# Optimization experiments

Hardware: AMD Instinct MI355X
Metric: run time of the kernel (lower is better)

## Reference

```python
import jax, jax.numpy as jnp
import numpy as np

EPS = 1e-5

@jax.custom_vjp
def sign_ste(x):
    # BinActivation / weight binarization: sign(x) in {-1,+1}
    return jnp.where(x >= 0, 1.0, -1.0).astype(x.dtype)

def _sign_fwd(x):
    return sign_ste(x), x

def _sign_bwd(x, g):
    # straight-through estimator with hardtanh clipping: pass grad where |x| <= 1
    return (g * (jnp.abs(x) <= 1.0).astype(g.dtype),)

sign_ste.defvjp(_sign_fwd, _sign_bwd)

def setup_inputs() -> dict:
    key = jax.random.key(0)
    k1, k2 = jax.random.split(key)
    x = jax.random.normal(k1, (32, 256, 56, 56), dtype=jnp.float32)
    W = jax.random.normal(k2, (256, 256, 3, 3), dtype=jnp.float32) * 0.1
    gamma = jnp.ones((256,), dtype=jnp.float32)
    beta = jnp.zeros((256,), dtype=jnp.float32)
    return {"x": x, "W": W, "gamma": gamma, "beta": beta}

def reference(x, W, gamma, beta):
    # binarize activation and weights to {-1,+1}
    xb = sign_ste(x)
    wb = sign_ste(W)
    # conv: NCHW x OIHW -> NCHW, stride 1, padding 1, dilation 1, no bias
    y = jax.lax.conv_general_dilated(
        xb, wb,
        window_strides=(1, 1),
        padding=[(1, 1), (1, 1)],
        rhs_dilation=(1, 1),
        dimension_numbers=("NCHW", "OIHW", "NCHW"),
    )
    # BatchNorm2d in training mode: batch statistics over (N,H,W), affine
    mean = jnp.mean(y, axis=(0, 2, 3), keepdims=True)          # [1,C,1,1]
    var = jnp.mean((y - mean) ** 2, axis=(0, 2, 3), keepdims=True)
    y = (y - mean) * jax.lax.rsqrt(var + EPS)
    y = y * gamma[None, :, None, None] + beta[None, :, None, None]
    # Hardtanh(-1, 1)
    return jnp.clip(y, -1.0, 1.0)
```

## Files before the change

### kernel.cpp

```cpp
#include <hip/hip_runtime.h>
#include <stdint.h>
#include <math.h>

#define N_IMG 32
#define C_IN  256
#define HW    56
#define P_PIX (HW*HW)
#define OC    256
#define WPC   8
#define NPIX  (N_IMG*P_PIX)
#define NTOT  ((double)N_IMG*(double)P_PIX)

__global__ __launch_bounds__(256) void pack_x_kernel(const float* __restrict__ x,
                                                     uint32_t* __restrict__ px,
                                                     uint32_t* __restrict__ zero_row) {
    if (blockIdx.x == 392) {
        if (threadIdx.x < 224) ((uint2*)zero_row)[threadIdx.x] = make_uint2(0u, 0u);
        return;
    }
    int lane = threadIdx.x & 63;
    int wh   = threadIdx.x >> 6;
    int pq   = blockIdx.x * 64 + lane;
    int n    = pq / 784;
    int q    = pq - n * 784;
    const float* xp = x + ((size_t)(n * C_IN + wh * 64)) * P_PIX + q * 4;
    uint32_t b0[4] = {0, 0, 0, 0};
    uint32_t b1[4] = {0, 0, 0, 0};
#pragma unroll 8
    for (int i = 0; i < 32; ++i) {
        float4 v = *(const float4*)(xp + (size_t)i * P_PIX);
        uint32_t bit = 1u << i;
        b0[0] |= (v.x >= 0.0f) ? bit : 0u;
        b0[1] |= (v.y >= 0.0f) ? bit : 0u;
        b0[2] |= (v.z >= 0.0f) ? bit : 0u;
        b0[3] |= (v.w >= 0.0f) ? bit : 0u;
    }
#pragma unroll 8
    for (int i = 0; i < 32; ++i) {
        float4 v = *(const float4*)(xp + (size_t)(i + 32) * P_PIX);
        uint32_t bit = 1u << i;
        b1[0] |= (v.x >= 0.0f) ? bit : 0u;
        b1[1] |= (v.y >= 0.0f) ? bit : 0u;
        b1[2] |= (v.z >= 0.0f) ? bit : 0u;
        b1[3] |= (v.w >= 0.0f) ? bit : 0u;
    }
    uint32_t* dst = px + ((size_t)(n * P_PIX + q * 4)) * WPC + wh * 2;
    *(uint2*)(dst + 0)  = make_uint2(b0[0], b1[0]);
    *(uint2*)(dst + 8)  = make_uint2(b0[1], b1[1]);
    *(uint2*)(dst + 16) = make_uint2(b0[2], b1[2]);
    *(uint2*)(dst + 24) = make_uint2(b0[3], b1[3]);
}

__global__ void pack_w_kernel(const float* __restrict__ Wt,
                              uint32_t* __restrict__ wp,
                              int* __restrict__ corr,
                              long long* __restrict__ sums,
                              long long* __restrict__ sumsq) {
    __shared__ int lpop[72];
    __shared__ int ltap[9];
    int o = blockIdx.x;
    int t = threadIdx.x;
    if (t == 0) { sums[o] = 0; sumsq[o] = 0; }
    if (t < 72) {
        int tap = t >> 3;
        int word = t & 7;
        const float* wpr = Wt + ((size_t)(o * C_IN + word * 32)) * 9 + tap;
        uint32_t bits = 0;
#pragma unroll
        for (int k = 0; k < 32; ++k) {
            float v = wpr[(size_t)k * 9];
            bits |= (v >= 0.0f) ? (1u << k) : 0u;
        }
        wp[o * 72 + t] = bits;
        lpop[t] = __popc(bits);
    }
    __syncthreads();
    if (t < 9) {
        int s = 0;
#pragma unroll
        for (int w = 0; w < 8; ++w) s += lpop[t * 8 + w];
        ltap[t] = s;
    }
    __syncthreads();
    if (t < 9) {
        int vc = t / 3, hc = t % 3;
        int c = 0;
        for (int dy = -1; dy <= 1; ++dy)
            for (int dx = -1; dx <= 1; ++dx) {
                bool inv = (dy == -1 && vc == 1) || (dy == 1 && vc == 2) ||
                           (dx == -1 && hc == 1) || (dx == 1 && hc == 2);
                if (inv) {
                    int tap = (dy + 1) * 3 + (dx + 1);
                    c += 256 - 2 * ltap[tap];
                }
            }
        corr[o * 9 + t] = c;
    }
}

#define LOADCOL(S, c) do {                                                    \
    int _c = (c);                                                             \
    const uint32_t* _p0 = ((unsigned)_c < 56u) ? (r0 + _c * 8) : zero_row;    \
    const uint32_t* _p1 = ((unsigned)_c < 56u) ? (r1 + _c * 8) : zero_row;    \
    const uint32_t* _p2 = ((unsigned)_c < 56u) ? (r2 + _c * 8) : zero_row;    \
    x0##S##a = *(const uint4*)_p0; x0##S##b = *(const uint4*)(_p0 + 4);       \
    x1##S##a = *(const uint4*)_p1; x1##S##b = *(const uint4*)(_p1 + 4);       \
    x2##S##a = *(const uint4*)_p2; x2##S##b = *(const uint4*)(_p2 + 4);       \
} while (0)

#define TAP(va, vb, t)                                                        \
    a0 += __popc((va).x ^ wreg[(t)*8+0]); a1 += __popc((va).y ^ wreg[(t)*8+1]); \
    a2 += __popc((va).z ^ wreg[(t)*8+2]); a3 += __popc((va).w ^ wreg[(t)*8+3]); \
    a0 += __popc((vb).x ^ wreg[(t)*8+4]); a1 += __popc((vb).y ^ wreg[(t)*8+5]); \
    a2 += __popc((vb).z ^ wreg[(t)*8+6]); a3 += __popc((vb).w ^ wreg[(t)*8+7]);

#define STEP(M, Cc, P, w, yptr) do {                                          \
    int a0 = 0, a1 = 0, a2 = 0, a3 = 0;                                       \
    TAP(x0##M##a,  x0##M##b,  0) TAP(x0##Cc##a, x0##Cc##b, 1) TAP(x0##P##a, x0##P##b, 2) \
    TAP(x1##M##a,  x1##M##b,  3) TAP(x1##Cc##a, x1##Cc##b, 4) TAP(x1##P##a, x1##P##b, 5) \
    TAP(x2##M##a,  x2##M##b,  6) TAP(x2##Cc##a, x2##Cc##b, 7) TAP(x2##P##a, x2##P##b, 8) \
    int acc = (a0 + a1) + (a2 + a3);                                          \
    int cr  = ((w) == 0) ? crL : (((w) == HW - 1) ? crR : crM);               \
    int v   = 2304 - 2 * acc - cr;                                            \
    *(yptr) = (short)v;                                                       \
    s += v; q += __mul24(v, v);                                               \
    LOADCOL(M, (w) + 3);                                                      \
} while (0)

__global__ __launch_bounds__(256, 2) void bconv_kernel(const uint32_t* __restrict__ px,
                                                       const uint32_t* __restrict__ wp,
                                                       const int* __restrict__ corr,
                                                       const uint32_t* __restrict__ zero_row,
                                                       short* __restrict__ y16t,
                                                       long long* __restrict__ sums,
                                                       long long* __restrict__ sumsq) {
    int o   = threadIdx.x;
    int blk = blockIdx.x;
    int n = blk / HW, h = blk - n * HW;

    uint32_t wreg[72];
    {
        const uint4* wq = (const uint4*)(wp + o * 72);
#pragma unroll
        for (int j = 0; j < 18; ++j) {
            uint4 t4 = wq[j];
            wreg[4*j+0] = t4.x; wreg[4*j+1] = t4.y;
            wreg[4*j+2] = t4.z; wreg[4*j+3] = t4.w;
        }
    }
    int vc  = (h == 0) ? 1 : ((h == HW - 1) ? 2 : 0);
    int crM = corr[o * 9 + vc * 3 + 0];
    int crL = corr[o * 9 + vc * 3 + 1];
    int crR = corr[o * 9 + vc * 3 + 2];

    const uint32_t* rowb = px + (size_t)(n * P_PIX) * WPC;
    const uint32_t* r0 = (h > 0)      ? rowb + (h - 1) * HW * WPC : zero_row;
    const uint32_t* r1 = rowb + h * HW * WPC;
    const uint32_t* r2 = (h < HW - 1) ? rowb + (h + 1) * HW * WPC : zero_row;

    uint4 x0Aa, x0Ab, x1Aa, x1Ab, x2Aa, x2Ab;
    uint4 x0Ba, x0Bb, x1Ba, x1Bb, x2Ba, x2Bb;
    uint4 x0Ca, x0Cb, x1Ca, x1Cb, x2Ca, x2Cb;
    uint4 x0Da, x0Db, x1Da, x1Db, x2Da, x2Db;

    LOADCOL(A, -1);
    LOADCOL(B, 0);
    LOADCOL(C, 1);
    LOADCOL(D, 2);

    short* yw = y16t + ((size_t)(n * P_PIX + h * HW)) * OC + o;
    int s = 0, q = 0;

    for (int wb = 0; wb < HW; wb += 4) {
        STEP(A, B, C, wb + 0, yw);
        STEP(B, C, D, wb + 1, yw + OC);
        STEP(C, D, A, wb + 2, yw + 2 * OC);
        STEP(D, A, B, wb + 3, yw + 3 * OC);
        yw += 4 * OC;
    }

    atomicAdd((unsigned long long*)&sums[o],  (unsigned long long)(long long)s);
    atomicAdd((unsigned long long*)&sumsq[o], (unsigned long long)(long long)q);
}

__global__ __launch_bounds__(256) void apply_kernel(const short* __restrict__ y16t,
                                                    float* __restrict__ out,
                                                    const long long* __restrict__ sums,
                                                    const long long* __restrict__ sumsq,
                                                    const float* __restrict__ gamma,
                                                    const float* __restrict__ beta) {
    __shared__ float sbf[512];
    __shared__ uint32_t tile[64 * 129];
    int t = threadIdx.x;
    {
        int o = t;
        double invN = 1.0 / NTOT;
        double mean = (double)sums[o] * invN;
        double var  = (double)sumsq[o] * invN - mean * mean;
        double sc   = (double)gamma[o] / sqrt(var + 1e-5);
        sbf[o]       = (float)sc;
        sbf[256 + o] = (float)((double)beta[o] - mean * sc);
    }
    int blk = blockIdx.x;
    int n   = blk / 49;
    int pl0 = (blk - n * 49) * 64;
    size_t P0 = (size_t)n * P_PIX + pl0;
#pragma unroll
    for (int r = 0; r < 8; ++r) {
        int f8  = r * 256 + t;
        int pxl = f8 >> 5;
        int c8  = f8 & 31;
        uint4 v = *(const uint4*)(y16t + (P0 + pxl) * OC + c8 * 8);
        uint32_t* d = &tile[pxl * 129 + c8 * 4];
        d[0] = v.x; d[1] = v.y; d[2] = v.z; d[3] = v.w;
    }
    __syncthreads();
    int lane = t & 63, wv = t >> 6;
    int lp = lane & 15, lc = lane >> 4;
    int px0 = lp * 4;
#pragma unroll
    for (int i = 0; i < 16; ++i) {
        int ch = i * 16 + wv * 4 + lc;
        float sc = sbf[ch], bi = sbf[256 + ch];
        int sh = (ch & 1) << 4;
        int ci = ch >> 1;
        float4 ov;
        {
            int v0 = (int)(short)(tile[(px0 + 0) * 129 + ci] >> sh);
            int v1 = (int)(short)(tile[(px0 + 1) * 129 + ci] >> sh);
            int v2 = (int)(short)(tile[(px0 + 2) * 129 + ci] >> sh);
            int v3 = (int)(short)(tile[(px0 + 3) * 129 + ci] >> sh);
            ov.x = fminf(fmaxf(fmaf((float)v0, sc, bi), -1.0f), 1.0f);
            ov.y = fminf(fmaxf(fmaf((float)v1, sc, bi), -1.0f), 1.0f);
            ov.z = fminf(fmaxf(fmaf((float)v2, sc, bi), -1.0f), 1.0f);
            ov.w = fminf(fmaxf(fmaf((float)v3, sc, bi), -1.0f), 1.0f);
        }
        *(float4*)(out + ((size_t)(n * OC + ch)) * P_PIX + pl0 + px0) = ov;
    }
}

extern "C" void kernel_launch(void* const* d_in, const int* in_sizes, int n_in,
                              void* d_out, int out_size, void* d_ws, size_t ws_size,
                              hipStream_t stream) {
    const float* x     = (const float*)d_in[0];
    const float* Wt    = (const float*)d_in[1];
    const float* gamma = (const float*)d_in[2];
    const float* beta  = (const float*)d_in[3];
    float* out = (float*)d_out;
    char* ws = (char*)d_ws;

    uint32_t*  px       = (uint32_t*) (ws);
    uint32_t*  wp       = (uint32_t*) (ws + 3211264);
    int*       corr     = (int*)      (ws + 3284992);
    long long* sums     = (long long*)(ws + 3294208);
    long long* sumsq    = (long long*)(ws + 3296256);
    uint32_t*  zero_row = (uint32_t*) (ws + 3298304);
    short*     y16t     = (short*)    (ws + 3300352);

    hipLaunchKernelGGL(pack_x_kernel, dim3(393),  dim3(256), 0, stream, x, px, zero_row);
    hipLaunchKernelGGL(pack_w_kernel, dim3(OC),   dim3(128), 0, stream, Wt, wp, corr, sums, sumsq);
    hipLaunchKernelGGL(bconv_kernel,  dim3(1792), dim3(256), 0, stream, px, wp, corr, zero_row,
                       y16t, sums, sumsq);
    hipLaunchKernelGGL(apply_kernel,  dim3(1568), dim3(256), 0, stream, y16t, out,
                       sums, sumsq, gamma, beta);
}
```

Before: 357.0 us.

## Stage packed input rows in LDS and peel boundary columns in bconv

Each block now cooperatively copies its three packed input rows, with zero-padded border columns, into shared memory once. Per-thread column loads then read broadcast LDS addresses instead of every thread issuing identical global loads. The width loop is also restructured to rotate three registers instead of four, with the first and last columns peeled so the boundary correction no longer needs a per-step select. This adds a barrier and about 5.5KB of LDS per block, which could affect occupancy at two blocks per CU.

New measurement: 337.4 us. 1.06x faster.

```diff
diff --git a/kernel.cpp b/kernel.cpp
--- a/kernel.cpp
+++ b/kernel.cpp
@@ -98,14 +98,12 @@
     }
 }
 
-#define LOADCOL(S, c) do {                                                    \
-    int _c = (c);                                                             \
-    const uint32_t* _p0 = ((unsigned)_c < 56u) ? (r0 + _c * 8) : zero_row;    \
-    const uint32_t* _p1 = ((unsigned)_c < 56u) ? (r1 + _c * 8) : zero_row;    \
-    const uint32_t* _p2 = ((unsigned)_c < 56u) ? (r2 + _c * 8) : zero_row;    \
-    x0##S##a = *(const uint4*)_p0; x0##S##b = *(const uint4*)(_p0 + 4);       \
-    x1##S##a = *(const uint4*)_p1; x1##S##b = *(const uint4*)(_p1 + 4);       \
-    x2##S##a = *(const uint4*)_p2; x2##S##b = *(const uint4*)(_p2 + 4);       \
+#define XS_COLS 58
+#define LOADCOL(S, cslot) do {                                                \
+    int _c2 = (cslot) * 2;                                                    \
+    x0##S##a = xs[0][_c2]; x0##S##b = xs[0][_c2 + 1];                         \
+    x1##S##a = xs[1][_c2]; x1##S##b = xs[1][_c2 + 1];                         \
+    x2##S##a = xs[2][_c2]; x2##S##b = xs[2][_c2 + 1];                         \
 } while (0)
 
 #define TAP(va, vb, t)                                                        \
@@ -114,17 +112,15 @@
     a0 += __popc((vb).x ^ wreg[(t)*8+4]); a1 += __popc((vb).y ^ wreg[(t)*8+5]); \
     a2 += __popc((vb).z ^ wreg[(t)*8+6]); a3 += __popc((vb).w ^ wreg[(t)*8+7]);
 
-#define STEP(M, Cc, P, w, yptr) do {                                          \
+#define STEP(M, Cc, P, cr, yptr) do {                                         \
     int a0 = 0, a1 = 0, a2 = 0, a3 = 0;                                       \
     TAP(x0##M##a,  x0##M##b,  0) TAP(x0##Cc##a, x0##Cc##b, 1) TAP(x0##P##a, x0##P##b, 2) \
     TAP(x1##M##a,  x1##M##b,  3) TAP(x1##Cc##a, x1##Cc##b, 4) TAP(x1##P##a, x1##P##b, 5) \
     TAP(x2##M##a,  x2##M##b,  6) TAP(x2##Cc##a, x2##Cc##b, 7) TAP(x2##P##a, x2##P##b, 8) \
     int acc = (a0 + a1) + (a2 + a3);                                          \
-    int cr  = ((w) == 0) ? crL : (((w) == HW - 1) ? crR : crM);               \
-    int v   = 2304 - 2 * acc - cr;                                            \
+    int v   = 2304 - 2 * acc - (cr);                                          \
     *(yptr) = (short)v;                                                       \
     s += v; q += __mul24(v, v);                                               \
-    LOADCOL(M, (w) + 3);                                                      \
 } while (0)
 
 __global__ __launch_bounds__(256, 2) void bconv_kernel(const uint32_t* __restrict__ px,
@@ -134,9 +130,31 @@
                                                        short* __restrict__ y16t,
                                                        long long* __restrict__ sums,
                                                        long long* __restrict__ sumsq) {
+    __shared__ uint4 xs[3][XS_COLS * 2];
     int o   = threadIdx.x;
     int blk = blockIdx.x;
     int n = blk / HW, h = blk - n * HW;
+
+    {
+        const uint32_t* rowb = px + (size_t)(n * P_PIX) * WPC;
+        const uint32_t* rsrc0 = (h > 0)      ? rowb + (h - 1) * HW * WPC : zero_row;
+        const uint32_t* rsrc1 = rowb + h * HW * WPC;
+        const uint32_t* rsrc2 = (h < HW - 1) ? rowb + (h + 1) * HW * WPC : zero_row;
+        for (int i = threadIdx.x; i < 348; i += 256) {
+            if (i < 336) {
+                int r  = i / 112;
+                int c4 = i - r * 112;
+                const uint32_t* src = (r == 0 ? rsrc0 : (r == 1 ? rsrc1 : rsrc2)) + c4 * 4;
+                xs[r][2 + c4] = *(const uint4*)src;
+            } else {
+                int j = i - 336;
+                int r = j >> 2;
+                int k = j & 3;
+                int idx = (k < 2) ? k : (57 * 2 + (k - 2));
+                xs[r][idx] = make_uint4(0u, 0u, 0u, 0u);
+            }
+        }
+    }
 
     uint32_t wreg[72];
     {
@@ -153,31 +171,28 @@
     int crL = corr[o * 9 + vc * 3 + 1];
     int crR = corr[o * 9 + vc * 3 + 2];
 
-    const uint32_t* rowb = px + (size_t)(n * P_PIX) * WPC;
-    const uint32_t* r0 = (h > 0)      ? rowb + (h - 1) * HW * WPC : zero_row;
-    const uint32_t* r1 = rowb + h * HW * WPC;
-    const uint32_t* r2 = (h < HW - 1) ? rowb + (h + 1) * HW * WPC : zero_row;
+    __syncthreads();
 
     uint4 x0Aa, x0Ab, x1Aa, x1Ab, x2Aa, x2Ab;
     uint4 x0Ba, x0Bb, x1Ba, x1Bb, x2Ba, x2Bb;
     uint4 x0Ca, x0Cb, x1Ca, x1Cb, x2Ca, x2Cb;
-    uint4 x0Da, x0Db, x1Da, x1Db, x2Da, x2Db;
-
-    LOADCOL(A, -1);
-    LOADCOL(B, 0);
-    LOADCOL(C, 1);
-    LOADCOL(D, 2);
 
     short* yw = y16t + ((size_t)(n * P_PIX + h * HW)) * OC + o;
     int s = 0, q = 0;
 
-    for (int wb = 0; wb < HW; wb += 4) {
-        STEP(A, B, C, wb + 0, yw);
-        STEP(B, C, D, wb + 1, yw + OC);
-        STEP(C, D, A, wb + 2, yw + 2 * OC);
-        STEP(D, A, B, wb + 3, yw + 3 * OC);
-        yw += 4 * OC;
-    }
+    LOADCOL(A, 0); LOADCOL(B, 1); LOADCOL(C, 2);
+    STEP(A, B, C, crL, yw);
+    LOADCOL(A, 3);
+    yw += OC;
+
+    for (int wb = 1; wb <= 52; wb += 3) {
+        STEP(B, C, A, crM, yw);          LOADCOL(B, wb + 3);
+        STEP(C, A, B, crM, yw + OC);     LOADCOL(C, wb + 4);
+        STEP(A, B, C, crM, yw + 2 * OC); LOADCOL(A, wb + 5);
+        yw += 3 * OC;
+    }
+
+    STEP(B, C, A, crR, yw);
 
     atomicAdd((unsigned long long*)&sums[o],  (unsigned long long)(long long)s);
     atomicAdd((unsigned long long*)&sumsq[o], (unsigned long long)(long long)q);
```
